# Optimization experiments

Hardware: AMD Instinct MI355X
Metric: run time of the kernel (lower is better)

Reference implementation:

```python
import jax, jax.numpy as jnp
import numpy as np

R = 50000          # residues
P = 24             # residue_pad_length
APR = 15           # atoms per residue (<= P)
N = R * APR        # total atoms
ACD = ATD = RCD = RID = 32
N_ATOM_CODES, N_ATOM_TYPES, N_RES_CODES, MAX_SEQ = 38, 6, 21, 1024
VEC_OUT, SC_OUT = 64, 256          # irreps_out = 64x1e + 256x0e
SC_IN = P * ACD + P * ATD + RCD + RID  # 1600 scalar inputs


def setup_inputs() -> dict:
    key = jax.random.key(0)
    ks = jax.random.split(key, 10)
    return {
        "residue_base_coords": jax.random.normal(ks[0], (R, 3), jnp.float32),
        "residue_relative_coords": jax.random.normal(ks[1], (N, 3), jnp.float32),
        "residue_code_index": jax.random.randint(ks[2], (R,), 0, N_RES_CODES),
        "residue_sequence_index": jnp.arange(R) % MAX_SEQ,
        "atom_code_index": jax.random.randint(ks[3], (N,), 0, N_ATOM_CODES),
        "atom_type_index": jax.random.randint(ks[4], (N,), 0, N_ATOM_TYPES),
        "residue_index_atomwise": jnp.repeat(jnp.arange(R), APR),  # sorted, APR atoms each
        "W_atom_code": jax.random.normal(ks[5], (N_ATOM_CODES, ACD), jnp.float32),
        "W_atom_type": jax.random.normal(ks[6], (N_ATOM_TYPES, ATD), jnp.float32),
        "W_res_code": jax.random.normal(ks[7], (N_RES_CODES, RCD), jnp.float32),
        "W_res_idx": jax.random.normal(ks[8], (MAX_SEQ, RID), jnp.float32),
        "W_vec": jax.random.normal(jax.random.fold_in(key, 1), (P, VEC_OUT), jnp.float32),
        "W_sc": jax.random.normal(ks[9], (SC_IN, SC_OUT), jnp.float32),
    }


def reference(residue_base_coords, residue_relative_coords, residue_code_index,
              residue_sequence_index, atom_code_index, atom_type_index,
              residue_index_atomwise, W_atom_code, W_atom_type, W_res_code,
              W_res_idx, W_vec, W_sc):
    R_ = residue_base_coords.shape[0]
    P_ = W_vec.shape[0]
    N_ = residue_index_atomwise.shape[0]
    ri = residue_index_atomwise
    # vectorized replacement of the per-residue python loop:
    # position of each atom within its residue (residue_index_atomwise is sorted)
    offsets = jnp.searchsorted(ri, jnp.arange(R_))            # first atom of each residue
    pos = jnp.arange(N_) - offsets[ri]                        # [N]
    # scatter atoms into padded [R, P, ...] layout (pad slots stay 0, like F.pad)
    mask = jnp.zeros((R_, P_), bool).at[ri, pos].set(True)
    rel = jnp.zeros((R_, P_, 3), residue_relative_coords.dtype).at[ri, pos].set(residue_relative_coords)
    codes = jnp.zeros((R_, P_), atom_code_index.dtype).at[ri, pos].set(atom_code_index)
    types = jnp.zeros((R_, P_), atom_type_index.dtype).at[ri, pos].set(atom_type_index)
    maskf = mask.astype(W_atom_code.dtype)[..., None]
    # embedding lookups, masked (pad embeddings zeroed as in the torch code)
    ac = (W_atom_code[codes] * maskf).reshape(R_, -1)         # [R, P*ACD]
    at = (W_atom_type[types] * maskf).reshape(R_, -1)         # [R, P*ATD]
    rc = W_res_code[residue_code_index]                       # [R, RCD]
    rix = W_res_idx[residue_sequence_index]                   # [R, RID]
    scalars = jnp.concatenate([ac, at, rc, rix], axis=-1)     # [R, SC_IN]
    # e3nn o3.Linear: l=1 channels mix only with l=1 (Px1e -> VEC_OUTx1e),
    # l=0 channels mix only with l=0; path-normalized by sqrt(fan_in), no bias.
    out_vec = jnp.einsum('rpc,pm->rmc', rel, W_vec) / jnp.sqrt(jnp.float32(P_))
    out_sc = (scalars @ W_sc) / jnp.sqrt(jnp.float32(scalars.shape[-1]))
    features = jnp.concatenate([out_vec.reshape(R_, -1), out_sc], axis=-1)  # [R, 3*VEC_OUT+SC_OUT]
    return residue_base_coords, features  # ResidueState(coords, features)
```

## Files before the change

kernel.cpp:

```cpp
#include <hip/hip_runtime.h>
#include <stdint.h>

static constexpr int P       = 24;
static constexpr int EMB_D   = 32;
static constexpr int N_AC    = 38;
static constexpr int N_AT    = 6;
static constexpr int N_RC    = 21;
static constexpr int MAXSEQ  = 1024;
static constexpr int VEC_OUT = 64;
static constexpr int SC_OUT  = 256;
static constexpr int FEAT    = 3 * VEC_OUT + SC_OUT;
static constexpr int CT      = N_AC * N_AT;
static constexpr int NROWS   = P * CT;
static constexpr int ROWB    = SC_OUT * 2;
static constexpr uint32_t ZROWB = (uint32_t)NROWS * ROWB;

__device__ __forceinline__ unsigned short f2bf(float f) {
    uint32_t x = __float_as_uint(f);
    uint32_t r = (x + 0x7FFFu + ((x >> 16) & 1u)) >> 16;
    return (unsigned short)r;
}

__global__ __launch_bounds__(256) void k1_init_build(
        const float* __restrict__ Wac, const float* __restrict__ Wat,
        const float* __restrict__ Wrc, const float* __restrict__ Wri,
        const float* __restrict__ Wsc,
        float* __restrict__ Ec, float* __restrict__ Et,
        float* __restrict__ Erc, float* __restrict__ Erix,
        int* __restrict__ starts, int* __restrict__ ends, int R) {
    int b = blockIdx.x;
    const int initB = (R + 255) / 256;
    if (b < initB) {
        int i = b * 256 + threadIdx.x;
        if (i < R) { starts[i] = 0; ends[i] = 0; }
        return;
    }
    b -= initB;
    const float* Wemb; float* E; int n_emb, sc_base, idx;
    if (b < P * N_AC) {
        Wemb = Wac; E = Ec; n_emb = N_AC; sc_base = 0; idx = b;
    } else if (b < P * N_AC + P * N_AT) {
        Wemb = Wat; E = Et; n_emb = N_AT; sc_base = P * EMB_D; idx = b - P * N_AC;
    } else if (b < P * N_AC + P * N_AT + N_RC) {
        Wemb = Wrc; E = Erc; n_emb = N_RC; sc_base = 2 * P * EMB_D;
        idx = b - (P * N_AC + P * N_AT);
    } else {
        Wemb = Wri; E = Erix; n_emb = MAXSEQ; sc_base = 2 * P * EMB_D + EMB_D;
        idx = b - (P * N_AC + P * N_AT + N_RC);
    }
    int p = idx / n_emb, e = idx % n_emb;
    int o = threadIdx.x;
    const float* wrow = Wemb + (size_t)e * EMB_D;
    const float* scol = Wsc + (size_t)(sc_base + p * EMB_D) * SC_OUT + o;
    float s = 0.f;
#pragma unroll
    for (int d = 0; d < EMB_D; ++d) s += wrow[d] * scol[(size_t)d * SC_OUT];
    E[(size_t)idx * SC_OUT + o] = s * 0.025f;
}

__global__ void k2_find_bounds(const int* __restrict__ ri, int* __restrict__ starts,
                               int* __restrict__ ends, int N) {
    int i = blockIdx.x * blockDim.x + threadIdx.x;
    if (i >= N) return;
    int r = ri[i];
    if (i == 0 || ri[i - 1] != r) starts[r] = i;
    if (i == N - 1 || ri[i + 1] != r) ends[r] = i + 1;
}

__global__ __launch_bounds__(256) void k3_fuse_hdr(
        const float* __restrict__ Ec, const float* __restrict__ Et,
        unsigned short* __restrict__ Etab,
        const int* __restrict__ starts, const int* __restrict__ ends,
        const int* __restrict__ rcode, const int* __restrict__ rseq,
        int4* __restrict__ hdr, int R) {
    int b = blockIdx.x;
    if (b < NROWS + 1) {
        int o = threadIdx.x;
        if (b == NROWS) { Etab[(size_t)b * SC_OUT + o] = 0; return; }
        int j = b / CT, ct = b % CT, c = ct / N_AT, t = ct % N_AT;
        float s = Ec[((size_t)j * N_AC + c) * SC_OUT + o] +
                  Et[((size_t)j * N_AT + t) * SC_OUT + o];
        Etab[(size_t)b * SC_OUT + o] = f2bf(s);
        return;
    }
    int i = (b - (NROWS + 1)) * 256 + threadIdx.x;
    if (i >= R) return;
    int st = starts[i];
    int c = ends[i] - st;
    if (c > P) c = P;
    hdr[i] = make_int4(st, c, rcode[i], rseq[i]);
}

__global__ __launch_bounds__(256) void k4_residue(
        const float* __restrict__ base, const int4* __restrict__ hdr,
        const int* __restrict__ acode, const int* __restrict__ atype,
        const float* __restrict__ rel, const unsigned char* __restrict__ tab,
        const float* __restrict__ Erc, const float* __restrict__ Erix,
        const float* __restrict__ Wvec,
        float* __restrict__ out_coords, float* __restrict__ out_feat,
        int R, int N) {
    __shared__ float lds_w[P * VEC_OUT];
    for (int t = threadIdx.x; t < P * VEC_OUT; t += 256) lds_w[t] = Wvec[t];
    __syncthreads();

    int wid = (blockIdx.x << 2) + (threadIdx.x >> 6);
    int lane = threadIdx.x & 63;
    int r = __builtin_amdgcn_readfirstlane(wid);
    if (r >= R) return;

    int4 h = hdr[r];
    const int off = h.x, cnt = h.y;

    int ia = off + lane; if (ia > N - 1) ia = N - 1;
    int code = acode[ia];
    int type = atype[ia];
    uint32_t rowoff = ZROWB;
    if (lane < cnt) rowoff = (uint32_t)((lane * CT + code * N_AT + type) * ROWB);
    int ir = 3 * off + lane; if (ir > 3 * N - 1) ir = 3 * N - 1;
    float relv = rel[ir];
    if (lane >= 3 * cnt) relv = 0.f;

    float4 ea = *reinterpret_cast<const float4*>(Erc + (size_t)h.z * SC_OUT + lane * 4);
    float4 eb = *reinterpret_cast<const float4*>(Erix + (size_t)h.w * SC_OUT + lane * 4);
    float a0 = ea.x + eb.x, a1 = ea.y + eb.y, a2 = ea.z + eb.z, a3 = ea.w + eb.w;
    float v0 = 0.f, v1 = 0.f, v2 = 0.f;
    const int lb = lane * 8;

    uint32_t ro[16];
#pragma unroll
    for (int k = 0; k < 16; ++k)
        ro[k] = (uint32_t)__builtin_amdgcn_readlane((int)rowoff, k);
    uint2 g[16];
#pragma unroll
    for (int k = 0; k < 16; ++k)
        g[k] = *reinterpret_cast<const uint2*>(tab + ro[k] + lb);

    float rx[16], ry[16], rz[16];
#pragma unroll
    for (int k = 0; k < 16; ++k) {
        rx[k] = __int_as_float(__builtin_amdgcn_readlane(__float_as_int(relv), 3 * k));
        ry[k] = __int_as_float(__builtin_amdgcn_readlane(__float_as_int(relv), 3 * k + 1));
        rz[k] = __int_as_float(__builtin_amdgcn_readlane(__float_as_int(relv), 3 * k + 2));
    }

#pragma unroll
    for (int k = 0; k < 16; ++k) {
        float w = lds_w[k * VEC_OUT + lane];
        a0 += __uint_as_float(g[k].x << 16);
        a1 += __uint_as_float(g[k].x & 0xFFFF0000u);
        a2 += __uint_as_float(g[k].y << 16);
        a3 += __uint_as_float(g[k].y & 0xFFFF0000u);
        v0 = fmaf(rx[k], w, v0);
        v1 = fmaf(ry[k], w, v1);
        v2 = fmaf(rz[k], w, v2);
    }

    if (cnt > 16) {
        int ir2 = 3 * off + 64 + lane;
        if (ir2 > 3 * N - 1) ir2 = 3 * N - 1;
        float relv2 = rel[ir2];
        if (64 + lane >= 3 * cnt) relv2 = 0.f;
#pragma unroll
        for (int k = 16; k < P; ++k) {
            uint32_t rr = (uint32_t)__builtin_amdgcn_readlane((int)rowoff, k);
            uint2 gg = *reinterpret_cast<const uint2*>(tab + rr + lb);
            float w = lds_w[k * VEC_OUT + lane];
            float sx = __int_as_float(3 * k < 64
                ? __builtin_amdgcn_readlane(__float_as_int(relv), 3 * k)
                : __builtin_amdgcn_readlane(__float_as_int(relv2), 3 * k - 64));
            float sy = __int_as_float(3 * k + 1 < 64
                ? __builtin_amdgcn_readlane(__float_as_int(relv), 3 * k + 1)
                : __builtin_amdgcn_readlane(__float_as_int(relv2), 3 * k + 1 - 64));
            float sz = __int_as_float(3 * k + 2 < 64
                ? __builtin_amdgcn_readlane(__float_as_int(relv), 3 * k + 2)
                : __builtin_amdgcn_readlane(__float_as_int(relv2), 3 * k + 2 - 64));
            a0 += __uint_as_float(gg.x << 16);
            a1 += __uint_as_float(gg.x & 0xFFFF0000u);
            a2 += __uint_as_float(gg.y << 16);
            a3 += __uint_as_float(gg.y & 0xFFFF0000u);
            v0 = fmaf(sx, w, v0);
            v1 = fmaf(sy, w, v1);
            v2 = fmaf(sz, w, v2);
        }
    }

    const float vs = 0.20412414523193150818f;
    float* frow = out_feat + (size_t)r * FEAT;
    frow[lane * 3 + 0] = v0 * vs;
    frow[lane * 3 + 1] = v1 * vs;
    frow[lane * 3 + 2] = v2 * vs;
    *reinterpret_cast<float4*>(frow + 3 * VEC_OUT + lane * 4) =
        make_float4(a0, a1, a2, a3);
    if (lane < 3) out_coords[(size_t)r * 3 + lane] = base[(size_t)r * 3 + lane];
}

extern "C" void kernel_launch(void* const* d_in, const int* in_sizes, int n_in,
                              void* d_out, int out_size, void* d_ws, size_t ws_size,
                              hipStream_t stream) {
    const float* base  = (const float*)d_in[0];
    const float* rel   = (const float*)d_in[1];
    const int*   rcode = (const int*)d_in[2];
    const int*   rseq  = (const int*)d_in[3];
    const int*   acode = (const int*)d_in[4];
    const int*   atype = (const int*)d_in[5];
    const int*   ri    = (const int*)d_in[6];
    const float* Wac   = (const float*)d_in[7];
    const float* Wat   = (const float*)d_in[8];
    const float* Wrc   = (const float*)d_in[9];
    const float* Wri   = (const float*)d_in[10];
    const float* Wv    = (const float*)d_in[11];
    const float* Wsc   = (const float*)d_in[12];

    const int R = in_sizes[0] / 3;
    const int N = in_sizes[6];

    float* out_coords = (float*)d_out;
    float* out_feat   = out_coords + (size_t)R * 3;

    char* ws = (char*)d_ws;
    size_t ofs = 0;
    auto alloc = [&](size_t bytes) {
        void* p = ws + ofs;
        ofs = (ofs + bytes + 255) & ~255ULL;
        return p;
    };
    int*            starts = (int*)alloc((size_t)R * 4);
    int*            ends   = (int*)alloc((size_t)R * 4);
    float*          Ec_f   = (float*)alloc((size_t)P * N_AC * SC_OUT * 4);
    float*          Et_f   = (float*)alloc((size_t)P * N_AT * SC_OUT * 4);
    float*          Erc_f  = (float*)alloc((size_t)N_RC * SC_OUT * 4);
    float*          Erix_f = (float*)alloc((size_t)MAXSEQ * SC_OUT * 4);
    unsigned short* Etab   = (unsigned short*)alloc((size_t)(NROWS + 1) * SC_OUT * 2);
    int4*           hdr    = (int4*)alloc((size_t)R * 16);
    (void)ws_size; (void)n_in; (void)out_size;

    const int initB = (R + 255) / 256;
    const int k1B   = initB + P * N_AC + P * N_AT + N_RC + MAXSEQ;
    const int hdrB  = (R + 255) / 256;
    const int k3B   = (NROWS + 1) + hdrB;

    k1_init_build<<<k1B, 256, 0, stream>>>(Wac, Wat, Wrc, Wri, Wsc,
                                           Ec_f, Et_f, Erc_f, Erix_f, starts, ends, R);
    k2_find_bounds<<<(N + 255) / 256, 256, 0, stream>>>(ri, starts, ends, N);
    k3_fuse_hdr<<<k3B, 256, 0, stream>>>(Ec_f, Et_f, Etab, starts, ends,
                                         rcode, rseq, hdr, R);
    k4_residue<<<(R + 3) / 4, 256, 0, stream>>>(
        base, hdr, acode, atype, rel, (const unsigned char*)Etab,
        Erc_f, Erix_f, Wv, out_coords, out_feat, R, N);
}
```

Before: 63.80 us.

## Precompute per-residue gather records and software-pipeline persistent residue kernel

The prep kernel now writes a 64-word record per residue holding precomputed table row offsets for the first 16 atoms and their relative coordinates. The main kernel becomes persistent with a fixed grid of 1024 blocks. Each wave loops over residues and double-buffers the header/record loads and table gathers, so the next residue's loads overlap the current residue's accumulation. The W_vec rows now live in registers instead of LDS. This is meant to hide gather latency, but it adds an extra global write and read of the record array (about 12.8 MB) and falls back to a slow scalar path for residues with more than 16 atoms.

```diff
diff --git a/kernel.cpp b/kernel.cpp
--- a/kernel.cpp
+++ b/kernel.cpp
@@ -67,12 +67,14 @@
     if (i == N - 1 || ri[i + 1] != r) ends[r] = i + 1;
 }
 
-__global__ __launch_bounds__(256) void k3_fuse_hdr(
+__global__ __launch_bounds__(256) void k3_fuse_prep(
         const float* __restrict__ Ec, const float* __restrict__ Et,
         unsigned short* __restrict__ Etab,
         const int* __restrict__ starts, const int* __restrict__ ends,
         const int* __restrict__ rcode, const int* __restrict__ rseq,
-        int4* __restrict__ hdr, int R) {
+        const int* __restrict__ acode, const int* __restrict__ atype,
+        const float* __restrict__ rel,
+        int4* __restrict__ hdr, uint32_t* __restrict__ recArr, int R) {
     int b = blockIdx.x;
     if (b < NROWS + 1) {
         int o = threadIdx.x;
@@ -83,115 +85,147 @@
         Etab[(size_t)b * SC_OUT + o] = f2bf(s);
         return;
     }
-    int i = (b - (NROWS + 1)) * 256 + threadIdx.x;
-    if (i >= R) return;
-    int st = starts[i];
-    int c = ends[i] - st;
-    if (c > P) c = P;
-    hdr[i] = make_int4(st, c, rcode[i], rseq[i]);
-}
-
-__global__ __launch_bounds__(256) void k4_residue(
+    b -= NROWS + 1;
+    const int hdrB = (R + 255) >> 8;
+    if (b < hdrB) {
+        int i = b * 256 + threadIdx.x;
+        if (i < R) {
+            int st = starts[i];
+            int c = ends[i] - st; if (c > P) c = P;
+            hdr[i] = make_int4(st, c, rcode[i], rseq[i]);
+        }
+        return;
+    }
+    b -= hdrB;
+    int i = b * 256 + threadIdx.x;
+    if (i >= R * 64) return;
+    int r = i >> 6, l = i & 63;
+    int st = starts[r];
+    int c = ends[r] - st; if (c > P) c = P;
+    uint32_t out;
+    if (l < 16) {
+        out = ZROWB;
+        if (l < c)
+            out = (uint32_t)((l * CT + acode[st + l] * N_AT + atype[st + l]) * ROWB);
+    } else {
+        int idx = l - 16, k = idx / 3, cc = idx - k * 3;
+        float v = 0.f;
+        if (k < c) v = rel[(size_t)(st + k) * 3 + cc];
+        out = __float_as_uint(v);
+    }
+    recArr[(size_t)r * 64 + l] = out;
+}
+
+__global__ __launch_bounds__(256, 4) void k4_residue(
         const float* __restrict__ base, const int4* __restrict__ hdr,
-        const int* __restrict__ acode, const int* __restrict__ atype,
-        const float* __restrict__ rel, const unsigned char* __restrict__ tab,
+        const uint32_t* __restrict__ recArr,
+        const unsigned char* __restrict__ tab,
         const float* __restrict__ Erc, const float* __restrict__ Erix,
         const float* __restrict__ Wvec,
-        float* __restrict__ out_coords, float* __restrict__ out_feat,
-        int R, int N) {
-    __shared__ float lds_w[P * VEC_OUT];
-    for (int t = threadIdx.x; t < P * VEC_OUT; t += 256) lds_w[t] = Wvec[t];
-    __syncthreads();
-
-    int wid = (blockIdx.x << 2) + (threadIdx.x >> 6);
-    int lane = threadIdx.x & 63;
-    int r = __builtin_amdgcn_readfirstlane(wid);
-    if (r >= R) return;
-
-    int4 h = hdr[r];
-    const int off = h.x, cnt = h.y;
-
-    int ia = off + lane; if (ia > N - 1) ia = N - 1;
-    int code = acode[ia];
-    int type = atype[ia];
-    uint32_t rowoff = ZROWB;
-    if (lane < cnt) rowoff = (uint32_t)((lane * CT + code * N_AT + type) * ROWB);
-    int ir = 3 * off + lane; if (ir > 3 * N - 1) ir = 3 * N - 1;
-    float relv = rel[ir];
-    if (lane >= 3 * cnt) relv = 0.f;
-
-    float4 ea = *reinterpret_cast<const float4*>(Erc + (size_t)h.z * SC_OUT + lane * 4);
-    float4 eb = *reinterpret_cast<const float4*>(Erix + (size_t)h.w * SC_OUT + lane * 4);
-    float a0 = ea.x + eb.x, a1 = ea.y + eb.y, a2 = ea.z + eb.z, a3 = ea.w + eb.w;
-    float v0 = 0.f, v1 = 0.f, v2 = 0.f;
-    const int lb = lane * 8;
-
-    uint32_t ro[16];
-#pragma unroll
-    for (int k = 0; k < 16; ++k)
-        ro[k] = (uint32_t)__builtin_amdgcn_readlane((int)rowoff, k);
-    uint2 g[16];
-#pragma unroll
-    for (int k = 0; k < 16; ++k)
-        g[k] = *reinterpret_cast<const uint2*>(tab + ro[k] + lb);
-
-    float rx[16], ry[16], rz[16];
-#pragma unroll
-    for (int k = 0; k < 16; ++k) {
-        rx[k] = __int_as_float(__builtin_amdgcn_readlane(__float_as_int(relv), 3 * k));
-        ry[k] = __int_as_float(__builtin_amdgcn_readlane(__float_as_int(relv), 3 * k + 1));
-        rz[k] = __int_as_float(__builtin_amdgcn_readlane(__float_as_int(relv), 3 * k + 2));
-    }
-
-#pragma unroll
-    for (int k = 0; k < 16; ++k) {
-        float w = lds_w[k * VEC_OUT + lane];
-        a0 += __uint_as_float(g[k].x << 16);
-        a1 += __uint_as_float(g[k].x & 0xFFFF0000u);
-        a2 += __uint_as_float(g[k].y << 16);
-        a3 += __uint_as_float(g[k].y & 0xFFFF0000u);
-        v0 = fmaf(rx[k], w, v0);
-        v1 = fmaf(ry[k], w, v1);
-        v2 = fmaf(rz[k], w, v2);
-    }
-
-    if (cnt > 16) {
-        int ir2 = 3 * off + 64 + lane;
-        if (ir2 > 3 * N - 1) ir2 = 3 * N - 1;
-        float relv2 = rel[ir2];
-        if (64 + lane >= 3 * cnt) relv2 = 0.f;
-#pragma unroll
-        for (int k = 16; k < P; ++k) {
-            uint32_t rr = (uint32_t)__builtin_amdgcn_readlane((int)rowoff, k);
-            uint2 gg = *reinterpret_cast<const uint2*>(tab + rr + lb);
-            float w = lds_w[k * VEC_OUT + lane];
-            float sx = __int_as_float(3 * k < 64
-                ? __builtin_amdgcn_readlane(__float_as_int(relv), 3 * k)
-                : __builtin_amdgcn_readlane(__float_as_int(relv2), 3 * k - 64));
-            float sy = __int_as_float(3 * k + 1 < 64
-                ? __builtin_amdgcn_readlane(__float_as_int(relv), 3 * k + 1)
-                : __builtin_amdgcn_readlane(__float_as_int(relv2), 3 * k + 1 - 64));
-            float sz = __int_as_float(3 * k + 2 < 64
-                ? __builtin_amdgcn_readlane(__float_as_int(relv), 3 * k + 2)
-                : __builtin_amdgcn_readlane(__float_as_int(relv2), 3 * k + 2 - 64));
-            a0 += __uint_as_float(gg.x << 16);
-            a1 += __uint_as_float(gg.x & 0xFFFF0000u);
-            a2 += __uint_as_float(gg.y << 16);
-            a3 += __uint_as_float(gg.y & 0xFFFF0000u);
-            v0 = fmaf(sx, w, v0);
-            v1 = fmaf(sy, w, v1);
-            v2 = fmaf(sz, w, v2);
-        }
-    }
-
-    const float vs = 0.20412414523193150818f;
-    float* frow = out_feat + (size_t)r * FEAT;
-    frow[lane * 3 + 0] = v0 * vs;
-    frow[lane * 3 + 1] = v1 * vs;
-    frow[lane * 3 + 2] = v2 * vs;
-    *reinterpret_cast<float4*>(frow + 3 * VEC_OUT + lane * 4) =
-        make_float4(a0, a1, a2, a3);
-    if (lane < 3) out_coords[(size_t)r * 3 + lane] = base[(size_t)r * 3 + lane];
+        const int* __restrict__ acode, const int* __restrict__ atype,
+        const float* __restrict__ rel,
+        float* __restrict__ out_coords, float* __restrict__ out_feat, int R) {
+
+    const int wave   = (blockIdx.x << 2) + (threadIdx.x >> 6);
+    const int lane   = threadIdx.x & 63;
+    const int lb     = lane * 8;
+    const int lane4  = lane * 4;
+    const int totalw = gridDim.x << 2;
+    const int NJ = (R + totalw - 1) / totalw;
+    const int J6 = (NJ / 6) * 6;
+
+    float w[16];
+#pragma unroll
+    for (int k = 0; k < 16; ++k) w[k] = Wvec[k * VEC_OUT + lane];
+
+    uint32_t rec0, rec1, rec2;
+    int4 h0, h1, h2;
+    uint2 gA[16], gB[16];
+    float4 eaA, ebA, eaB, ebB;
+
+    auto RAW = [&](uint32_t& RB, int4& HB, int jj) {
+        int rr = wave + jj * totalw;
+        rr = rr < R ? rr : R - 1;
+        HB = hdr[rr];
+        RB = recArr[(size_t)rr * 64 + lane];
+    };
+    auto GATHER = [&](uint2 (&G)[16], float4& EA, float4& EB,
+                      uint32_t RB, const int4& HB) {
+#pragma unroll
+        for (int k = 0; k < 16; ++k) {
+            uint32_t ro = (uint32_t)__builtin_amdgcn_readlane((int)RB, k);
+            G[k] = *reinterpret_cast<const uint2*>(tab + ro + lb);
+        }
+        EA = *reinterpret_cast<const float4*>(Erc + (size_t)HB.z * SC_OUT + lane4);
+        EB = *reinterpret_cast<const float4*>(Erix + (size_t)HB.w * SC_OUT + lane4);
+    };
+    auto ACC = [&](const uint2 (&G)[16], const float4& EA, const float4& EB,
+                   uint32_t RB, const int4& HB, int jj) {
+        int rr = wave + jj * totalw;
+        if (rr >= R) return;
+        float a0 = EA.x + EB.x, a1 = EA.y + EB.y;
+        float a2 = EA.z + EB.z, a3 = EA.w + EB.w;
+        float v0 = 0.f, v1 = 0.f, v2 = 0.f;
+#pragma unroll
+        for (int k = 0; k < 16; ++k) {
+            a0 += __uint_as_float(G[k].x << 16);
+            a1 += __uint_as_float(G[k].x & 0xFFFF0000u);
+            a2 += __uint_as_float(G[k].y << 16);
+            a3 += __uint_as_float(G[k].y & 0xFFFF0000u);
+            float sx = __uint_as_float((uint32_t)__builtin_amdgcn_readlane((int)RB, 16 + 3 * k));
+            float sy = __uint_as_float((uint32_t)__builtin_amdgcn_readlane((int)RB, 17 + 3 * k));
+            float sz = __uint_as_float((uint32_t)__builtin_amdgcn_readlane((int)RB, 18 + 3 * k));
+            v0 = fmaf(sx, w[k], v0);
+            v1 = fmaf(sy, w[k], v1);
+            v2 = fmaf(sz, w[k], v2);
+        }
+        int cnt = HB.y;
+        if (cnt > 16) {
+            int st = HB.x;
+            for (int k = 16; k < cnt; ++k) {
+                int c = acode[st + k], t = atype[st + k];
+                uint32_t ro = (uint32_t)((k * CT + c * N_AT + t) * ROWB);
+                uint2 gg = *reinterpret_cast<const uint2*>(tab + ro + lb);
+                float ww = Wvec[k * VEC_OUT + lane];
+                a0 += __uint_as_float(gg.x << 16);
+                a1 += __uint_as_float(gg.x & 0xFFFF0000u);
+                a2 += __uint_as_float(gg.y << 16);
+                a3 += __uint_as_float(gg.y & 0xFFFF0000u);
+                float sx = rel[(size_t)(st + k) * 3];
+                float sy = rel[(size_t)(st + k) * 3 + 1];
+                float sz = rel[(size_t)(st + k) * 3 + 2];
+                v0 = fmaf(sx, ww, v0);
+                v1 = fmaf(sy, ww, v1);
+                v2 = fmaf(sz, ww, v2);
+            }
+        }
+        const float vs = 0.20412414523193150818f;
+        float* frow = out_feat + (size_t)rr * FEAT;
+        frow[lane * 3 + 0] = v0 * vs;
+        frow[lane * 3 + 1] = v1 * vs;
+        frow[lane * 3 + 2] = v2 * vs;
+        *reinterpret_cast<float4*>(frow + 3 * VEC_OUT + lane4) =
+            make_float4(a0, a1, a2, a3);
+        if (lane < 3) out_coords[(size_t)rr * 3 + lane] = base[(size_t)rr * 3 + lane];
+    };
+
+    RAW(rec0, h0, 0);
+    RAW(rec1, h1, 1);
+    GATHER(gA, eaA, ebA, rec0, h0);
+
+    for (int s = 0; s < J6; s += 6) {
+        RAW(rec2, h2, s + 2); GATHER(gB, eaB, ebB, rec1, h1); ACC(gA, eaA, ebA, rec0, h0, s + 0);
+        RAW(rec0, h0, s + 3); GATHER(gA, eaA, ebA, rec2, h2); ACC(gB, eaB, ebB, rec1, h1, s + 1);
+        RAW(rec1, h1, s + 4); GATHER(gB, eaB, ebB, rec0, h0); ACC(gA, eaA, ebA, rec2, h2, s + 2);
+        RAW(rec2, h2, s + 5); GATHER(gA, eaA, ebA, rec1, h1); ACC(gB, eaB, ebB, rec0, h0, s + 3);
+        RAW(rec0, h0, s + 6); GATHER(gB, eaB, ebB, rec2, h2); ACC(gA, eaA, ebA, rec1, h1, s + 4);
+        RAW(rec1, h1, s + 7); GATHER(gA, eaA, ebA, rec0, h0); ACC(gB, eaB, ebB, rec2, h2, s + 5);
+    }
+    for (int j = J6; j < NJ; ++j) {
+        RAW(rec0, h0, j);
+        GATHER(gA, eaA, ebA, rec0, h0);
+        ACC(gA, eaA, ebA, rec0, h0, j);
+    }
 }
 
 extern "C" void kernel_launch(void* const* d_in, const int* in_sizes, int n_in,
@@ -232,19 +266,21 @@
     float*          Erix_f = (float*)alloc((size_t)MAXSEQ * SC_OUT * 4);
     unsigned short* Etab   = (unsigned short*)alloc((size_t)(NROWS + 1) * SC_OUT * 2);
     int4*           hdr    = (int4*)alloc((size_t)R * 16);
+    uint32_t*       recArr = (uint32_t*)alloc((size_t)R * 64 * 4);
     (void)ws_size; (void)n_in; (void)out_size;
 
     const int initB = (R + 255) / 256;
     const int k1B   = initB + P * N_AC + P * N_AT + N_RC + MAXSEQ;
     const int hdrB  = (R + 255) / 256;
-    const int k3B   = (NROWS + 1) + hdrB;
+    const int recB  = (R * 64 + 255) / 256;
+    const int k3B   = (NROWS + 1) + hdrB + recB;
 
     k1_init_build<<<k1B, 256, 0, stream>>>(Wac, Wat, Wrc, Wri, Wsc,
                                            Ec_f, Et_f, Erc_f, Erix_f, starts, ends, R);
     k2_find_bounds<<<(N + 255) / 256, 256, 0, stream>>>(ri, starts, ends, N);
-    k3_fuse_hdr<<<k3B, 256, 0, stream>>>(Ec_f, Et_f, Etab, starts, ends,
-                                         rcode, rseq, hdr, R);
-    k4_residue<<<(R + 3) / 4, 256, 0, stream>>>(
-        base, hdr, acode, atype, rel, (const unsigned char*)Etab,
-        Erc_f, Erix_f, Wv, out_coords, out_feat, R, N);
-}
+    k3_fuse_prep<<<k3B, 256, 0, stream>>>(Ec_f, Et_f, Etab, starts, ends,
+                                          rcode, rseq, acode, atype, rel, hdr, recArr, R);
+    k4_residue<<<1024, 256, 0, stream>>>(
+        base, hdr, recArr, (const unsigned char*)Etab,
+        Erc_f, Erix_f, Wv, acode, atype, rel, out_coords, out_feat, R);
+}
```

After: 151.0 us. +136.7%, slower.
